# Kernel optimization log

Hardware: AMD Instinct MI355X
Metric: run time of the kernel (lower is better)

Reference implementation:

```python
import jax, jax.numpy as jnp
from jax import lax
import numpy as np

T, INPUT, RES, OUT = 4096, 64, 4096, 32
SPECTRAL_RADIUS, CONNECTIVITY = 0.9, 0.3


def setup_inputs() -> dict:
    key = jax.random.key(0)
    k_in, k_w, k_mask, k_x, k_out = jax.random.split(key, 5)
    inputs = jax.random.normal(k_x, (T, INPUT), dtype=jnp.float32)
    # W_in, W ~ U(-1, 1), as in (rand - 0.5) * 2
    W_in = jax.random.uniform(k_in, (RES, INPUT), minval=-1.0, maxval=1.0, dtype=jnp.float32)
    W = jax.random.uniform(k_w, (RES, RES), minval=-1.0, maxval=1.0, dtype=jnp.float32)
    mask = (jax.random.uniform(k_mask, (RES, RES)) < CONNECTIVITY).astype(jnp.float32)
    W = W * mask
    # rescale to spectral radius (done once at init; numpy eig on host)
    max_eig = np.max(np.abs(np.linalg.eigvals(np.asarray(W))))
    W = W / jnp.float32(max_eig / SPECTRAL_RADIUS)
    # trained readout (stand-in for pinv-solved W_out)
    W_out = jax.random.normal(k_out, (RES, OUT), dtype=jnp.float32) * 0.05
    return {"inputs": inputs, "W_in": W_in, "W": W, "W_out": W_out}


def reference(inputs, W_in, W, W_out):
    # X[:, 0] = 0; X[:, t] = tanh(W_in @ inputs[t] + W @ X[:, t-1]) for t >= 1
    u = inputs @ W_in.T  # [T, RES] precomputed input projections

    def step(x_prev, u_t):
        x_t = jnp.tanh(u_t + W @ x_prev)
        return x_t, x_t

    x0 = jnp.zeros((RES,), dtype=inputs.dtype)
    _, xs = lax.scan(step, x0, u[1:])  # [T-1, RES]
    X = jnp.concatenate([x0[None, :], xs], axis=0)  # [T, RES] == original X.T
    return X @ W_out  # [T, OUT]
```

## Files before the change

### kernel.cpp

```cpp
#include <hip/hip_runtime.h>
#include <hip/hip_fp16.h>

#define T_STEPS 4096
#define RES     4096
#define NIN     64
#define NOUT    32
#define NWG     256
#define TPB     512
#define WS      4168

typedef unsigned long long ull;
typedef _Float16 h2 __attribute__((ext_vector_type(2)));

__device__ __forceinline__ bool rdy(ull q) {
    return (__uint_as_float((unsigned)q) > 0.5f) &&
           (__uint_as_float((unsigned)(q >> 32)) > 0.5f);
}

__device__ __forceinline__ float dot8(uint4 wq, uint4 xq, float acc) {
    acc = __builtin_amdgcn_fdot2(__builtin_bit_cast(h2, wq.x), __builtin_bit_cast(h2, xq.x), acc, false);
    acc = __builtin_amdgcn_fdot2(__builtin_bit_cast(h2, wq.y), __builtin_bit_cast(h2, xq.y), acc, false);
    acc = __builtin_amdgcn_fdot2(__builtin_bit_cast(h2, wq.z), __builtin_bit_cast(h2, xq.z), acc, false);
    acc = __builtin_amdgcn_fdot2(__builtin_bit_cast(h2, wq.w), __builtin_bit_cast(h2, xq.w), acc, false);
    return acc;
}

__global__ void esn_init(float* __restrict__ Xf) {
    int i = blockIdx.x * 256 + threadIdx.x;
    if (i < RES) Xf[i] = 2.0f;
}

__global__ __launch_bounds__(TPB, 1)
void esn_recur(const float* __restrict__ inp,
               const float* __restrict__ Win,
               const float* __restrict__ W,
               float* __restrict__ Xf)
{
    __shared__ __align__(16) __half Wl[16 * WS];
    __shared__ __align__(16) __half xh[RES + NIN];
    __shared__ float red[16 * 33];

    const int g    = blockIdx.x;
    const int tid  = threadIdx.x;
    const int wv   = tid >> 6;
    const int lane = tid & 63;

    {
        const float4* Wg = (const float4*)(W + (size_t)g * 16 * RES);
        for (int idx = tid; idx < 16 * RES / 4; idx += TPB) {
            float4 v  = Wg[idx];
            int  row  = idx >> 10;
            int  c    = (idx & 1023) * 4;
            __half* d = &Wl[row * WS + c];
            d[0] = __float2half_rn(v.x);
            d[1] = __float2half_rn(v.y);
            d[2] = __float2half_rn(v.z);
            d[3] = __float2half_rn(v.w);
        }
        for (int idx = tid; idx < 16 * NIN; idx += TPB) {
            int row = idx >> 6, k = idx & 63;
            Wl[row * WS + RES + k] = __float2half_rn(Win[(size_t)(g * 16 + row) * NIN + k]);
        }
    }

    float u_cur = 0.f;
    if (tid < NIN) u_cur = inp[NIN + tid];

    __syncthreads();

    const uint4* WQ = (const uint4*)Wl;
    const uint4* XQ = (const uint4*)xh;
    const int r  = lane & 15;
    const int cg = lane >> 4;
    const int wb = r * (WS / 8) + wv * 64 + cg * 16;
    const int xb = wv * 64 + cg * 16;

    for (int t = 1; t < T_STEPS; ++t) {
        const ull* src = (const ull*)(Xf + (size_t)(t - 1) * RES) + tid * 4;
        ull q0 = 0, q1 = 0, q2 = 0, q3 = 0;
        int need = 15;
        do {
            if (need & 1) { q0 = __hip_atomic_load(src + 0, __ATOMIC_RELAXED, __HIP_MEMORY_SCOPE_AGENT); if (rdy(q0)) need &= ~1; }
            if (need & 2) { q1 = __hip_atomic_load(src + 1, __ATOMIC_RELAXED, __HIP_MEMORY_SCOPE_AGENT); if (rdy(q1)) need &= ~2; }
            if (need & 4) { q2 = __hip_atomic_load(src + 2, __ATOMIC_RELAXED, __HIP_MEMORY_SCOPE_AGENT); if (rdy(q2)) need &= ~4; }
            if (need & 8) { q3 = __hip_atomic_load(src + 3, __ATOMIC_RELAXED, __HIP_MEMORY_SCOPE_AGENT); if (rdy(q3)) need &= ~8; }
        } while (need);

        {
            __half hv[8];
            hv[0] = __float2half_rn(__uint_as_float((unsigned)q0)         - 2.0f);
            hv[1] = __float2half_rn(__uint_as_float((unsigned)(q0 >> 32)) - 2.0f);
            hv[2] = __float2half_rn(__uint_as_float((unsigned)q1)         - 2.0f);
            hv[3] = __float2half_rn(__uint_as_float((unsigned)(q1 >> 32)) - 2.0f);
            hv[4] = __float2half_rn(__uint_as_float((unsigned)q2)         - 2.0f);
            hv[5] = __float2half_rn(__uint_as_float((unsigned)(q2 >> 32)) - 2.0f);
            hv[6] = __float2half_rn(__uint_as_float((unsigned)q3)         - 2.0f);
            hv[7] = __float2half_rn(__uint_as_float((unsigned)(q3 >> 32)) - 2.0f);
            ((uint4*)xh)[tid] = *(const uint4*)hv;
        }
        if (tid < NIN) {
            xh[RES + tid] = __float2half_rn(u_cur);
            if (t + 1 < T_STEPS) u_cur = inp[(size_t)(t + 1) * NIN + tid];
        }

        __syncthreads();

        float acc = 0.f;
#pragma unroll
        for (int i = 0; i < 16; ++i)
            acc = dot8(WQ[wb + i], XQ[xb + i], acc);
        if (cg == 0)
            acc = dot8(WQ[r * (WS / 8) + RES / 8 + wv], XQ[RES / 8 + wv], acc);
        red[r * 33 + wv * 4 + cg] = acc;

        __syncthreads();

        if (wv == 0) {
            const int rr = lane >> 2, q = lane & 3;
            const float* rp = &red[rr * 33 + 8 * q];
            float s = ((rp[0] + rp[1]) + (rp[2] + rp[3])) +
                      ((rp[4] + rp[5]) + (rp[6] + rp[7]));
            s += __shfl_xor(s, 1, 64);
            s += __shfl_xor(s, 2, 64);
            if (q == 0) {
                float xn = tanhf(s);
                __hip_atomic_store(Xf + (size_t)t * RES + g * 16 + rr, xn + 2.0f,
                                   __ATOMIC_RELAXED, __HIP_MEMORY_SCOPE_AGENT);
            }
        }
    }
}

__global__ __launch_bounds__(256)
void esn_out(const float* __restrict__ Xf,
             const float* __restrict__ Wout,
             float* __restrict__ out)
{
    __shared__ float xs[2 * RES];
    __shared__ float red[2][8][32];
    const int tid = threadIdx.x;
    const int t0  = blockIdx.x * 2;

    const float4* s4 = (const float4*)(Xf + (size_t)t0 * RES);
    float4*       d4 = (float4*)xs;
    for (int i = tid; i < 2 * RES / 4; i += 256) {
        float4 v = s4[i];
        v.x -= 2.0f; v.y -= 2.0f; v.z -= 2.0f; v.w -= 2.0f;
        d4[i] = v;
    }
    __syncthreads();

    const int o  = tid & 31;
    const int sg = tid >> 5;
    float acc0 = 0.f, acc1 = 0.f;
    const int rbeg = sg * 512;
    for (int rr = rbeg; rr < rbeg + 512; ++rr) {
        float wv = Wout[(size_t)rr * NOUT + o];
        acc0 += xs[rr] * wv;
        acc1 += xs[RES + rr] * wv;
    }
    red[0][sg][o] = acc0;
    red[1][sg][o] = acc1;
    __syncthreads();

    if (tid < 64) {
        const int h = tid >> 5, oo = tid & 31;
        float s = 0.f;
#pragma unroll
        for (int k = 0; k < 8; ++k) s += red[h][k][oo];
        out[(size_t)(t0 + h) * NOUT + oo] = s;
    }
}

extern "C" void kernel_launch(void* const* d_in, const int* in_sizes, int n_in,
                              void* d_out, int out_size, void* d_ws, size_t ws_size,
                              hipStream_t stream)
{
    const float* inputs = (const float*)d_in[0];
    const float* W_in   = (const float*)d_in[1];
    const float* W      = (const float*)d_in[2];
    const float* W_out  = (const float*)d_in[3];
    float* out = (float*)d_out;

    float* Xf = (float*)d_ws;

    hipMemsetAsync(Xf, 0, (size_t)T_STEPS * RES * sizeof(float), stream);
    esn_init<<<dim3((RES + 255) / 256), dim3(256), 0, stream>>>(Xf);

    esn_recur<<<dim3(NWG), dim3(TPB), 0, stream>>>(inputs, W_in, W, Xf);
    esn_out<<<dim3(T_STEPS / 2), dim3(256), 0, stream>>>(Xf, W_out, out);
}
```

Before: 12.02 ms.

## Exchange reservoir state as fp16 and restructure per-step reduction and sync

The global state exchange between workgroups moves from fp32 to fp16-encoded values offset by 2, which halves polling traffic per step and lets one thread publish two rows in a single 32-bit atomic store. Weight fragments are preloaded into registers before the spin-wait with rotated indexing, so LDS reads overlap the wait and bank conflicts are reduced. One __syncthreads is replaced with an lgkmcnt wait, and the reduction buffer is double-buffered so all waves share the final reduction via shuffles. This relies on each wave reading only the x slice it wrote itself, and it lowers the precision of the stored history used by the readout.

```diff
diff --git a/kernel.cpp b/kernel.cpp
--- a/kernel.cpp
+++ b/kernel.cpp
@@ -8,42 +8,51 @@
 #define NWG     256
 #define TPB     512
 #define WS      4168
+#define WR      (WS / 8)
 
 typedef unsigned long long ull;
-typedef _Float16 h2 __attribute__((ext_vector_type(2)));
-
-__device__ __forceinline__ bool rdy(ull q) {
-    return (__uint_as_float((unsigned)q) > 0.5f) &&
-           (__uint_as_float((unsigned)(q >> 32)) > 0.5f);
-}
+typedef _Float16 hv2 __attribute__((ext_vector_type(2)));
 
 __device__ __forceinline__ float dot8(uint4 wq, uint4 xq, float acc) {
-    acc = __builtin_amdgcn_fdot2(__builtin_bit_cast(h2, wq.x), __builtin_bit_cast(h2, xq.x), acc, false);
-    acc = __builtin_amdgcn_fdot2(__builtin_bit_cast(h2, wq.y), __builtin_bit_cast(h2, xq.y), acc, false);
-    acc = __builtin_amdgcn_fdot2(__builtin_bit_cast(h2, wq.z), __builtin_bit_cast(h2, xq.z), acc, false);
-    acc = __builtin_amdgcn_fdot2(__builtin_bit_cast(h2, wq.w), __builtin_bit_cast(h2, xq.w), acc, false);
+    acc = __builtin_amdgcn_fdot2(__builtin_bit_cast(hv2, wq.x), __builtin_bit_cast(hv2, xq.x), acc, false);
+    acc = __builtin_amdgcn_fdot2(__builtin_bit_cast(hv2, wq.y), __builtin_bit_cast(hv2, xq.y), acc, false);
+    acc = __builtin_amdgcn_fdot2(__builtin_bit_cast(hv2, wq.z), __builtin_bit_cast(hv2, xq.z), acc, false);
+    acc = __builtin_amdgcn_fdot2(__builtin_bit_cast(hv2, wq.w), __builtin_bit_cast(hv2, xq.w), acc, false);
     return acc;
 }
 
-__global__ void esn_init(float* __restrict__ Xf) {
+__device__ __forceinline__ bool ok4(ull q) {
+    return ((unsigned short)q) && ((unsigned short)(q >> 16)) &&
+           ((unsigned short)(q >> 32)) && ((unsigned short)(q >> 48));
+}
+
+__device__ __forceinline__ unsigned sub2(unsigned u) {
+    __half2 h = *(__half2*)&u;
+    __half2 r = __hsub2(h, __floats2half2_rn(2.f, 2.f));
+    return *(unsigned*)&r;
+}
+
+__global__ void esn_init(unsigned short* __restrict__ Xh) {
     int i = blockIdx.x * 256 + threadIdx.x;
-    if (i < RES) Xf[i] = 2.0f;
+    if (i < RES) Xh[i] = 0x4000;
 }
 
 __global__ __launch_bounds__(TPB, 1)
 void esn_recur(const float* __restrict__ inp,
                const float* __restrict__ Win,
                const float* __restrict__ W,
-               float* __restrict__ Xf)
+               unsigned short* __restrict__ Xh)
 {
     __shared__ __align__(16) __half Wl[16 * WS];
     __shared__ __align__(16) __half xh[RES + NIN];
-    __shared__ float red[16 * 33];
+    __shared__ float red[2][16][33];
 
     const int g    = blockIdx.x;
     const int tid  = threadIdx.x;
     const int wv   = tid >> 6;
     const int lane = tid & 63;
+    const int r    = lane & 15;
+    const int cg   = lane >> 4;
 
     {
         const float4* Wg = (const float4*)(W + (size_t)g * 16 * RES);
@@ -63,68 +72,71 @@
         }
     }
 
-    float u_cur = 0.f;
-    if (tid < NIN) u_cur = inp[NIN + tid];
+    float u_cur = (wv == 0) ? inp[NIN + lane] : 0.f;
 
     __syncthreads();
 
-    const uint4* WQ = (const uint4*)Wl;
-    const uint4* XQ = (const uint4*)xh;
-    const int r  = lane & 15;
-    const int cg = lane >> 4;
-    const int wb = r * (WS / 8) + wv * 64 + cg * 16;
-    const int xb = wv * 64 + cg * 16;
+    const uint4* WQ    = (const uint4*)Wl;
+    const uint4* XQ    = (const uint4*)xh;
+    const int    wbase = r * WR + wv * 64 + 16 * cg;
+    const int    xbase = wv * 64 + 16 * cg;
 
     for (int t = 1; t < T_STEPS; ++t) {
-        const ull* src = (const ull*)(Xf + (size_t)(t - 1) * RES) + tid * 4;
-        ull q0 = 0, q1 = 0, q2 = 0, q3 = 0;
-        int need = 15;
+        uint4 wq[16];
+#pragma unroll
+        for (int i = 0; i < 16; ++i)
+            wq[i] = WQ[wbase + ((i + 4 * cg) & 15)];
+        uint4 wu0, wu1;
+        if (wv == 0) {
+            wu0 = WQ[r * WR + 512 + 2 * cg];
+            wu1 = WQ[r * WR + 513 + 2 * cg];
+        }
+        asm volatile("s_waitcnt lgkmcnt(0)" ::: "memory");
+
+        const ull* src = (const ull*)(Xh + (size_t)(t - 1) * RES) + 128 * wv + 2 * lane;
+        ull q0 = 0, q1 = 0;
+        int need = 3;
         do {
-            if (need & 1) { q0 = __hip_atomic_load(src + 0, __ATOMIC_RELAXED, __HIP_MEMORY_SCOPE_AGENT); if (rdy(q0)) need &= ~1; }
-            if (need & 2) { q1 = __hip_atomic_load(src + 1, __ATOMIC_RELAXED, __HIP_MEMORY_SCOPE_AGENT); if (rdy(q1)) need &= ~2; }
-            if (need & 4) { q2 = __hip_atomic_load(src + 2, __ATOMIC_RELAXED, __HIP_MEMORY_SCOPE_AGENT); if (rdy(q2)) need &= ~4; }
-            if (need & 8) { q3 = __hip_atomic_load(src + 3, __ATOMIC_RELAXED, __HIP_MEMORY_SCOPE_AGENT); if (rdy(q3)) need &= ~8; }
+            if (need & 1) { q0 = __hip_atomic_load(src,     __ATOMIC_RELAXED, __HIP_MEMORY_SCOPE_AGENT); if (ok4(q0)) need &= ~1; }
+            if (need & 2) { q1 = __hip_atomic_load(src + 1, __ATOMIC_RELAXED, __HIP_MEMORY_SCOPE_AGENT); if (ok4(q1)) need &= ~2; }
         } while (need);
 
-        {
-            __half hv[8];
-            hv[0] = __float2half_rn(__uint_as_float((unsigned)q0)         - 2.0f);
-            hv[1] = __float2half_rn(__uint_as_float((unsigned)(q0 >> 32)) - 2.0f);
-            hv[2] = __float2half_rn(__uint_as_float((unsigned)q1)         - 2.0f);
-            hv[3] = __float2half_rn(__uint_as_float((unsigned)(q1 >> 32)) - 2.0f);
-            hv[4] = __float2half_rn(__uint_as_float((unsigned)q2)         - 2.0f);
-            hv[5] = __float2half_rn(__uint_as_float((unsigned)(q2 >> 32)) - 2.0f);
-            hv[6] = __float2half_rn(__uint_as_float((unsigned)q3)         - 2.0f);
-            hv[7] = __float2half_rn(__uint_as_float((unsigned)(q3 >> 32)) - 2.0f);
-            ((uint4*)xh)[tid] = *(const uint4*)hv;
-        }
-        if (tid < NIN) {
-            xh[RES + tid] = __float2half_rn(u_cur);
-            if (t + 1 < T_STEPS) u_cur = inp[(size_t)(t + 1) * NIN + tid];
-        }
-
-        __syncthreads();
+        uint4 sv;
+        sv.x = sub2((unsigned)q0); sv.y = sub2((unsigned)(q0 >> 32));
+        sv.z = sub2((unsigned)q1); sv.w = sub2((unsigned)(q1 >> 32));
+        *(uint4*)(xh + 512 * wv + 8 * lane) = sv;
+        if (wv == 0) xh[RES + lane] = __float2half_rn(u_cur);
+        asm volatile("s_waitcnt lgkmcnt(0)" ::: "memory");
 
         float acc = 0.f;
 #pragma unroll
-        for (int i = 0; i < 16; ++i)
-            acc = dot8(WQ[wb + i], XQ[xb + i], acc);
-        if (cg == 0)
-            acc = dot8(WQ[r * (WS / 8) + RES / 8 + wv], XQ[RES / 8 + wv], acc);
-        red[r * 33 + wv * 4 + cg] = acc;
-
+        for (int i = 0; i < 16; ++i) {
+            uint4 xq = XQ[xbase + ((i + 4 * cg) & 15)];
+            acc = dot8(wq[i], xq, acc);
+        }
+        if (wv == 0) {
+            const uint4* XU = (const uint4*)(xh + RES);
+            acc = dot8(wu0, XU[2 * cg], acc);
+            acc = dot8(wu1, XU[2 * cg + 1], acc);
+            u_cur = (t + 1 < T_STEPS) ? inp[(size_t)(t + 1) * NIN + lane] : 0.f;
+        }
+        red[t & 1][r][4 * wv + cg] = acc;
         __syncthreads();
 
-        if (wv == 0) {
-            const int rr = lane >> 2, q = lane & 3;
-            const float* rp = &red[rr * 33 + 8 * q];
-            float s = ((rp[0] + rp[1]) + (rp[2] + rp[3])) +
-                      ((rp[4] + rp[5]) + (rp[6] + rp[7]));
+        {
+            const int row = 2 * wv + (lane >> 5);
+            float s = red[t & 1][row][lane & 31];
             s += __shfl_xor(s, 1, 64);
             s += __shfl_xor(s, 2, 64);
-            if (q == 0) {
-                float xn = tanhf(s);
-                __hip_atomic_store(Xf + (size_t)t * RES + g * 16 + rr, xn + 2.0f,
+            s += __shfl_xor(s, 4, 64);
+            s += __shfl_xor(s, 8, 64);
+            s += __shfl_xor(s, 16, 64);
+            float xn = tanhf(s);
+            unsigned enc = (unsigned)__half_as_ushort(__float2half_rn(xn + 2.0f));
+            unsigned hi  = (unsigned)__shfl((int)enc, 32, 64);
+            if (lane == 0) {
+                unsigned pk = enc | (hi << 16);
+                __hip_atomic_store((unsigned*)(Xh + (size_t)t * RES + 16 * g + 2 * wv), pk,
                                    __ATOMIC_RELAXED, __HIP_MEMORY_SCOPE_AGENT);
             }
         }
@@ -132,7 +144,7 @@
 }
 
 __global__ __launch_bounds__(256)
-void esn_out(const float* __restrict__ Xf,
+void esn_out(const unsigned short* __restrict__ Xh,
              const float* __restrict__ Wout,
              float* __restrict__ out)
 {
@@ -141,12 +153,15 @@
     const int tid = threadIdx.x;
     const int t0  = blockIdx.x * 2;
 
-    const float4* s4 = (const float4*)(Xf + (size_t)t0 * RES);
-    float4*       d4 = (float4*)xs;
-    for (int i = tid; i < 2 * RES / 4; i += 256) {
-        float4 v = s4[i];
-        v.x -= 2.0f; v.y -= 2.0f; v.z -= 2.0f; v.w -= 2.0f;
-        d4[i] = v;
+    const uint4* s4 = (const uint4*)(Xh + (size_t)t0 * RES);
+    for (int i = tid; i < 2 * RES / 8; i += 256) {
+        uint4 v  = s4[i];
+        float* d = &xs[8 * i];
+        float2 f;
+        f = __half22float2(*(__half2*)&v.x); d[0] = f.x - 2.f; d[1] = f.y - 2.f;
+        f = __half22float2(*(__half2*)&v.y); d[2] = f.x - 2.f; d[3] = f.y - 2.f;
+        f = __half22float2(*(__half2*)&v.z); d[4] = f.x - 2.f; d[5] = f.y - 2.f;
+        f = __half22float2(*(__half2*)&v.w); d[6] = f.x - 2.f; d[7] = f.y - 2.f;
     }
     __syncthreads();
 
@@ -182,11 +197,11 @@
     const float* W_out  = (const float*)d_in[3];
     float* out = (float*)d_out;
 
-    float* Xf = (float*)d_ws;
-
-    hipMemsetAsync(Xf, 0, (size_t)T_STEPS * RES * sizeof(float), stream);
-    esn_init<<<dim3((RES + 255) / 256), dim3(256), 0, stream>>>(Xf);
-
-    esn_recur<<<dim3(NWG), dim3(TPB), 0, stream>>>(inputs, W_in, W, Xf);
-    esn_out<<<dim3(T_STEPS / 2), dim3(256), 0, stream>>>(Xf, W_out, out);
-}
+    unsigned short* Xh = (unsigned short*)d_ws;
+
+    hipMemsetAsync(Xh, 0, (size_t)T_STEPS * RES * sizeof(unsigned short), stream);
+    esn_init<<<dim3((RES + 255) / 256), dim3(256), 0, stream>>>(Xh);
+
+    esn_recur<<<dim3(NWG), dim3(TPB), 0, stream>>>(inputs, W_in, W, Xh);
+    esn_out<<<dim3(T_STEPS / 2), dim3(256), 0, stream>>>(Xh, W_out, out);
+}
```

New measurement: 11.86 ms. No clear change (-1.3%).
